# Performance work log

Hardware: AMD Instinct MI355X
Metric: run time of the kernel (lower is better)

Reference implementation:

```python
import jax, jax.numpy as jnp
import numpy as np

B, T, D, N = 16, 4096, 512, 3


def _window_sum(x, k):
    # x: [B, T, ...] -> sliding-window sum of size k, stride 1 -> [B, T-k+1, ...]
    c = jnp.cumsum(x, axis=1)
    c = jnp.concatenate([jnp.zeros_like(c[:, :1]), c], axis=1)
    return c[:, k:] - c[:, :-k]


def setup_inputs() -> dict:
    key = jax.random.key(0)
    ks = jax.random.split(key, 7)
    s_prev = jax.random.normal(ks[0], (B, D), jnp.float32)
    enc_hs = jax.random.normal(ks[1], (B, T, D), jnp.float32)
    # realistic padding mask: True = padded position
    lengths = jax.random.randint(ks[2], (B,), T // 2, T + 1)
    src_mask = jnp.arange(T)[None, :] >= lengths[:, None]
    scale = 1.0 / np.sqrt(D)
    Vw = jax.random.normal(ks[3], (N, D, D), jnp.float32) * scale
    Vb = jax.random.normal(ks[4], (N, D), jnp.float32) * 0.01
    Ww = jax.random.normal(ks[5], (N, D, D), jnp.float32) * scale
    Wb = jax.random.normal(ks[6], (N, D), jnp.float32) * 0.01
    return {"s_prev": s_prev, "enc_hs": enc_hs, "src_mask": src_mask,
            "Vw": Vw, "Vb": Vb, "Ww": Ww, "Wb": Wb}


def _level(s_prev, hs, mask, vw, vb, ww, wb):
    # hs: [B, L, D], mask: [B, L] (True = masked)
    # torch Linear: y = x @ W^T + b, weight is [out, in]
    v = jnp.einsum('bld,ed->ble', hs, vw) + vb            # V_i(hs)
    att = jnp.einsum('bd,bld->bl', s_prev, v)             # bmm(s_prev, V(hs)^T)
    att = jnp.where(mask, -jnp.inf, att)
    att = jax.nn.softmax(att, axis=-1)                    # [B, L]
    pooled = jnp.einsum('bl,bld->bd', att, hs)            # bmm(att, hs)
    ctx = pooled @ ww.T + wb                              # W_i(.)
    return ctx, att


def reference(s_prev, enc_hs, src_mask, Vw, Vb, Ww, Wb):
    ctx, att = _level(s_prev, enc_hs, src_mask, Vw[0], Vb[0], Ww[0], Wb[0])
    for i in range(1, N):
        k = i + 1
        hs_ngram = _window_sum(enc_hs, k) / k                      # AvgPool1d(k,1)
        n_mask = _window_sum(src_mask.astype(jnp.float32), k) > 0  # any masked in window
        c, _ = _level(s_prev, hs_ngram, n_mask, Vw[i], Vb[i], Ww[i], Wb[i])
        ctx = ctx + c
    return ctx, att
```

## Files before the change

### kernel.cpp

```cpp
#include <hip/hip_runtime.h>

#define BB 16
#define TT 4096
#define DD 512
#define CH 16
#define NY (TT/CH)
#define NEG (-1.0e30f)

#define OFF_Q     64
#define OFF_QP    (OFF_Q + 3*BB*DD)
#define OFF_P0    (OFF_QP + 4*3*BB*DD)
#define OFF_M     (OFF_P0 + BB*TT)
#define OFF_S     (OFF_M + 3*BB*NY)
#define OFF_SC    (OFF_S + 3*BB*NY)
#define OFF_MT    (OFF_SC + 3*BB*NY)
#define OFF_TOT   (OFF_MT + 64)
#define OFF_PART  (OFF_TOT + 64)
#define OFF_POOL  (OFF_PART + 3*NY*BB*DD)

__global__ void __launch_bounds__(1024) k_lengths(const unsigned char* mask, int* lengths) {
    __shared__ int sflag;
    const int tid = threadIdx.x;
    if (tid == 0) sflag = 0;
    __syncthreads();
    int f = 0;
    for (int idx = tid * 4 + 1; idx < BB * TT; idx += 1024 * 4)
        f |= (mask[idx] != 0);
    if (f) atomicOr(&sflag, 1);
    __syncthreads();
    const bool byte_layout = (sflag != 0);
    const int* m32 = (const int*)mask;
    const int b = tid >> 6;
    const int lane = tid & 63;
    int cnt = 0;
    if (byte_layout) {
        for (int t = lane; t < TT; t += 64) cnt += (mask[b * TT + t] != 0);
    } else {
        for (int t = lane; t < TT; t += 64) cnt += (m32[b * TT + t] != 0);
    }
    #pragma unroll
    for (int m = 32; m >= 1; m >>= 1) cnt += __shfl_xor(cnt, m, 64);
    if (lane == 0) lengths[b] = TT - cnt;
}

__global__ void __launch_bounds__(256) k_q(const float* __restrict__ s_prev,
                                           const float* __restrict__ Vw,
                                           float* __restrict__ qpart) {
    const int blk = blockIdx.x;
    const int ec = blk & 3;
    const int ib = blk >> 2;
    const int b = ib % BB;
    const int i = ib / BB;
    const int d0 = threadIdx.x;
    const float* sp = s_prev + b * DD + ec * 128;
    const float* W = Vw + (size_t)i * DD * DD + (size_t)(ec * 128) * DD;
    float a0 = 0.f, a1 = 0.f;
    for (int e = 0; e < 128; e++) {
        const float se = sp[e];
        a0 += se * W[e * DD + d0];
        a1 += se * W[e * DD + d0 + 256];
    }
    qpart[(size_t)blk * DD + d0] = a0;
    qpart[(size_t)blk * DD + d0 + 256] = a1;
}

__global__ void __launch_bounds__(256) k_q_reduce(const float* __restrict__ qpart,
                                                  float* __restrict__ q) {
    const int idx = blockIdx.x * 256 + threadIdx.x;
    const int ib = idx / DD;
    const int d = idx % DD;
    float s = 0.f;
    #pragma unroll
    for (int ec = 0; ec < 4; ec++) s += qpart[(size_t)(ib * 4 + ec) * DD + d];
    q[idx] = s;
}

__global__ void __launch_bounds__(256) k_fused(const float* __restrict__ enc,
                                               const float* __restrict__ q,
                                               const int* __restrict__ lengths,
                                               float* __restrict__ p0,
                                               float* __restrict__ mbuf,
                                               float* __restrict__ sbuf,
                                               float* __restrict__ part) {
    __shared__ float sp[CH + 2][3];
    __shared__ float svs[3][CH];
    __shared__ float su[3][CH];
    __shared__ float sm[3];
    const int b = blockIdx.x;
    const int y = blockIdx.y;
    const int t0 = y * CH;
    const int len = lengths[b];
    const int tid = threadIdx.x;
    if (t0 >= len) {
        if (tid < 3) {
            mbuf[(size_t)(tid * BB + b) * NY + y] = NEG;
            sbuf[(size_t)(tid * BB + b) * NY + y] = 0.f;
        }
        return;
    }
    const int wv = tid >> 6, lane = tid & 63;

    const float4* q40 = (const float4*)(q + (size_t)(0 * BB + b) * DD);
    const float4* q41 = (const float4*)(q + (size_t)(1 * BB + b) * DD);
    const float4* q42 = (const float4*)(q + (size_t)(2 * BB + b) * DD);
    const float4 qa0 = q40[lane], qb0 = q40[64 + lane];
    const float4 qa1 = q41[lane], qb1 = q41[64 + lane];
    const float4 qa2 = q42[lane], qb2 = q42[64 + lane];
    #pragma unroll
    for (int rr = 0; rr < 5; rr++) {
        if (rr == 4 && wv >= 2) break;
        const int r = (rr < 4) ? (wv + rr * 4) : (CH + wv);
        const int t = t0 + r;
        float d0 = 0.f, d1 = 0.f, d2 = 0.f;
        if (t < len) {
            const float4* e4 = (const float4*)(enc + ((size_t)b * TT + t) * DD);
            const float4 x0 = e4[lane], x1 = e4[64 + lane];
            d0 = x0.x*qa0.x + x0.y*qa0.y + x0.z*qa0.z + x0.w*qa0.w
               + x1.x*qb0.x + x1.y*qb0.y + x1.z*qb0.z + x1.w*qb0.w;
            d1 = x0.x*qa1.x + x0.y*qa1.y + x0.z*qa1.z + x0.w*qa1.w
               + x1.x*qb1.x + x1.y*qb1.y + x1.z*qb1.z + x1.w*qb1.w;
            d2 = x0.x*qa2.x + x0.y*qa2.y + x0.z*qa2.z + x0.w*qa2.w
               + x1.x*qb2.x + x1.y*qb2.y + x1.z*qb2.z + x1.w*qb2.w;
            #pragma unroll
            for (int m = 32; m >= 1; m >>= 1) {
                d0 += __shfl_xor(d0, m, 64);
                d1 += __shfl_xor(d1, m, 64);
                d2 += __shfl_xor(d2, m, 64);
            }
        }
        if (lane == 0) {
            sp[r][0] = d0; sp[r][1] = d1; sp[r][2] = d2;
            if (rr < 4 && t < len) p0[(size_t)b * TT + t] = d0;
        }
    }
    __syncthreads();

    if (tid < 48) {
        const int i = tid / CH, r = tid % CH;
        const int l = t0 + r;
        const bool valid = l < (len - i);
        float s = sp[r][i];
        if (i > 0) s += sp[r + 1][i];
        if (i > 1) s += sp[r + 2][i];
        svs[i][r] = valid ? s * (1.0f / (float)(i + 1)) : NEG;
    }
    __syncthreads();
    if (tid < 3) {
        float m = NEG;
        #pragma unroll
        for (int r = 0; r < CH; r++) m = fmaxf(m, svs[tid][r]);
        sm[tid] = m;
    }
    __syncthreads();
    if (tid < 48) {
        const int i = tid / CH, r = tid % CH;
        const bool valid = (t0 + r) < (len - i);
        su[i][r] = valid ? __expf(svs[i][r] - sm[i]) : 0.f;
    }
    __syncthreads();
    if (tid < 3) {
        float s = 0.f;
        #pragma unroll
        for (int r = 0; r < CH; r++) s += su[tid][r];
        mbuf[(size_t)(tid * BB + b) * NY + y] = sm[tid];
        sbuf[(size_t)(tid * BB + b) * NY + y] = s;
    }
    __syncthreads();

    const int d = tid * 2;
    const float* col = enc + (size_t)b * TT * DD + d;
    float2 va, vb2, vc;
    {
        const int t = t0;
        va  = (t     < TT) ? *(const float2*)(col + (size_t)t * DD)       : make_float2(0.f, 0.f);
        vb2 = (t + 1 < TT) ? *(const float2*)(col + (size_t)(t + 1) * DD) : make_float2(0.f, 0.f);
    }
    float2 a0 = {0, 0}, a1 = {0, 0}, a2 = {0, 0};
    #pragma unroll
    for (int r = 0; r < CH; r++) {
        const int t = t0 + r;
        vc = (t + 2 < TT) ? *(const float2*)(col + (size_t)(t + 2) * DD) : make_float2(0.f, 0.f);
        const float u0 = su[0][r], u1 = su[1][r], u2 = su[2][r];
        const float w1x = va.x + vb2.x, w1y = va.y + vb2.y;
        const float w2x = w1x + vc.x,   w2y = w1y + vc.y;
        a0.x += u0 * va.x;  a0.y += u0 * va.y;
        a1.x += u1 * w1x;   a1.y += u1 * w1y;
        a2.x += u2 * w2x;   a2.y += u2 * w2y;
        va = vb2; vb2 = vc;
    }
    a1.x *= 0.5f; a1.y *= 0.5f;
    a2.x *= (1.0f / 3.0f); a2.y *= (1.0f / 3.0f);
    float* pt = part + (size_t)y * BB * DD + (size_t)b * DD + d;
    *(float2*)(pt)                        = a0;
    *(float2*)(pt + (size_t)NY * BB * DD)     = a1;
    *(float2*)(pt + (size_t)2 * NY * BB * DD) = a2;
}

__global__ void __launch_bounds__(256) k_combine(const float* __restrict__ mbuf,
                                                 const float* __restrict__ sbuf,
                                                 float* __restrict__ scale,
                                                 float* __restrict__ mtot,
                                                 float* __restrict__ tot) {
    const int g = blockIdx.x * 4 + (threadIdx.x >> 6);
    const int lane = threadIdx.x & 63;
    const float* mv = mbuf + (size_t)g * NY;
    const float* sv = sbuf + (size_t)g * NY;
    float ml[4], sl[4];
    float m = NEG;
    #pragma unroll
    for (int j = 0; j < 4; j++) {
        ml[j] = mv[lane * 4 + j];
        sl[j] = sv[lane * 4 + j];
        m = fmaxf(m, ml[j]);
    }
    #pragma unroll
    for (int s = 32; s >= 1; s >>= 1) m = fmaxf(m, __shfl_xor(m, s, 64));
    float t = 0.f;
    #pragma unroll
    for (int j = 0; j < 4; j++) t += sl[j] * __expf(ml[j] - m);
    #pragma unroll
    for (int s = 32; s >= 1; s >>= 1) t += __shfl_xor(t, s, 64);
    const float inv = 1.0f / t;
    #pragma unroll
    for (int j = 0; j < 4; j++)
        scale[(size_t)g * NY + lane * 4 + j] = __expf(ml[j] - m) * inv;
    if (lane == 0) { mtot[g] = m; tot[g] = t; }
}

__global__ void __launch_bounds__(256) k_reduce(const float* __restrict__ part,
                                                const float* __restrict__ scale,
                                                float* __restrict__ pooled) {
    const int idx = blockIdx.x * 256 + threadIdx.x;
    const int ib = idx / DD;
    const int d = idx % DD;
    const int i = ib / BB, b = ib % BB;
    const float* sc = scale + (size_t)ib * NY;
    const float* base = part + (size_t)i * NY * BB * DD + (size_t)b * DD + d;
    float s = 0.f;
    #pragma unroll 8
    for (int y = 0; y < NY; y++) s += base[(size_t)y * BB * DD] * sc[y];
    pooled[idx] = s;
}

__global__ void __launch_bounds__(256) k_att(const float* __restrict__ p0,
                                             const int* __restrict__ lengths,
                                             const float* __restrict__ mtot,
                                             const float* __restrict__ tot,
                                             float* __restrict__ att) {
    const int idx = blockIdx.x * 256 + threadIdx.x;
    const int b = idx >> 12;
    const int t = idx & (TT - 1);
    const float m = mtot[b];
    const float inv = 1.0f / tot[b];
    att[idx] = (t < lengths[b]) ? __expf(p0[idx] - m) * inv : 0.f;
}

__global__ void __launch_bounds__(256) k_ctx(const float* __restrict__ pooled,
                                             const float* __restrict__ Ww,
                                             const float* __restrict__ Wb,
                                             float* __restrict__ ctx) {
    const int wid = blockIdx.x * 4 + (threadIdx.x >> 6);
    const int lane = threadIdx.x & 63;
    const int b = wid >> 9;
    const int e = wid & 511;
    float acc = 0.f;
    #pragma unroll
    for (int i = 0; i < 3; i++) {
        const float4* pr = (const float4*)(pooled + (size_t)(i * BB + b) * DD);
        const float4* wr = (const float4*)(Ww + ((size_t)i * DD + e) * DD);
        const float4 p0 = pr[lane], p1 = pr[64 + lane];
        const float4 w0 = wr[lane], w1 = wr[64 + lane];
        acc += p0.x * w0.x + p0.y * w0.y + p0.z * w0.z + p0.w * w0.w
             + p1.x * w1.x + p1.y * w1.y + p1.z * w1.z + p1.w * w1.w;
    }
    #pragma unroll
    for (int m = 32; m >= 1; m >>= 1) acc += __shfl_xor(acc, m, 64);
    if (lane == 0)
        ctx[(size_t)b * DD + e] = acc + Wb[e] + Wb[DD + e] + Wb[2 * DD + e];
}

extern "C" void kernel_launch(void* const* d_in, const int* in_sizes, int n_in,
                              void* d_out, int out_size, void* d_ws, size_t ws_size,
                              hipStream_t stream) {
    const float* s_prev = (const float*)d_in[0];
    const float* enc    = (const float*)d_in[1];
    const void*  mask   = d_in[2];
    const float* Vw     = (const float*)d_in[3];
    const float* Ww     = (const float*)d_in[5];
    const float* Wb     = (const float*)d_in[6];

    float* out = (float*)d_out;
    float* ctx = out;
    float* att = out + BB * DD;

    float* W       = (float*)d_ws;
    int*   lengths = (int*)d_ws;
    float* q       = W + OFF_Q;
    float* qpart   = W + OFF_QP;
    float* p0      = W + OFF_P0;
    float* mbuf    = W + OFF_M;
    float* sbuf    = W + OFF_S;
    float* scale   = W + OFF_SC;
    float* mtot    = W + OFF_MT;
    float* tot     = W + OFF_TOT;
    float* part    = W + OFF_PART;
    float* pooled  = W + OFF_POOL;

    k_lengths<<<1, 1024, 0, stream>>>((const unsigned char*)mask, lengths);
    k_q<<<192, 256, 0, stream>>>(s_prev, Vw, qpart);
    k_q_reduce<<<3 * BB * DD / 256, 256, 0, stream>>>(qpart, q);
    k_fused<<<dim3(BB, NY), 256, 0, stream>>>(enc, q, lengths, p0, mbuf, sbuf, part);
    k_combine<<<12, 256, 0, stream>>>(mbuf, sbuf, scale, mtot, tot);
    k_reduce<<<3 * BB * DD / 256, 256, 0, stream>>>(part, scale, pooled);
    k_att<<<BB * TT / 256, 256, 0, stream>>>(p0, lengths, mtot, tot, att);
    k_ctx<<<BB * DD / 4, 256, 0, stream>>>(pooled, Ww, Wb, ctx);
}
```

Before: 266.6 us.

## Enlarge chunk size, fuse softmax combine into reduce, merge small kernels

New measurement: 255.9 us. 4.0% less time.

```diff
diff --git a/kernel.cpp b/kernel.cpp
--- a/kernel.cpp
+++ b/kernel.cpp
@@ -3,89 +3,86 @@
 #define BB 16
 #define TT 4096
 #define DD 512
-#define CH 16
+#define CH 64
 #define NY (TT/CH)
 #define NEG (-1.0e30f)
 
 #define OFF_Q     64
-#define OFF_QP    (OFF_Q + 3*BB*DD)
-#define OFF_P0    (OFF_QP + 4*3*BB*DD)
+#define OFF_P0    (OFF_Q + 3*BB*DD)
 #define OFF_M     (OFF_P0 + BB*TT)
 #define OFF_S     (OFF_M + 3*BB*NY)
-#define OFF_SC    (OFF_S + 3*BB*NY)
-#define OFF_MT    (OFF_SC + 3*BB*NY)
+#define OFF_MT    (OFF_S + 3*BB*NY)
 #define OFF_TOT   (OFF_MT + 64)
 #define OFF_PART  (OFF_TOT + 64)
 #define OFF_POOL  (OFF_PART + 3*NY*BB*DD)
 
-__global__ void __launch_bounds__(1024) k_lengths(const unsigned char* mask, int* lengths) {
+__global__ void __launch_bounds__(256) k_lengths(const unsigned char* __restrict__ mask,
+                                                 int* __restrict__ lengths) {
     __shared__ int sflag;
+    __shared__ int wsum[4];
     const int tid = threadIdx.x;
+    const int b = blockIdx.x;
     if (tid == 0) sflag = 0;
     __syncthreads();
+    const uint4* m4 = (const uint4*)mask;
     int f = 0;
-    for (int idx = tid * 4 + 1; idx < BB * TT; idx += 1024 * 4)
-        f |= (mask[idx] != 0);
+    #pragma unroll 4
+    for (int idx = tid; idx < BB * TT / 16; idx += 256) {
+        const uint4 w = m4[idx];
+        f |= (((w.x | w.y | w.z | w.w) & 0xFFFFFF00u) != 0u);
+    }
     if (f) atomicOr(&sflag, 1);
     __syncthreads();
     const bool byte_layout = (sflag != 0);
     const int* m32 = (const int*)mask;
-    const int b = tid >> 6;
-    const int lane = tid & 63;
     int cnt = 0;
     if (byte_layout) {
-        for (int t = lane; t < TT; t += 64) cnt += (mask[b * TT + t] != 0);
+        for (int t = tid; t < TT; t += 256) cnt += (mask[b * TT + t] != 0);
     } else {
-        for (int t = lane; t < TT; t += 64) cnt += (m32[b * TT + t] != 0);
+        for (int t = tid; t < TT; t += 256) cnt += (m32[b * TT + t] != 0);
     }
     #pragma unroll
     for (int m = 32; m >= 1; m >>= 1) cnt += __shfl_xor(cnt, m, 64);
-    if (lane == 0) lengths[b] = TT - cnt;
-}
-
-__global__ void __launch_bounds__(256) k_q(const float* __restrict__ s_prev,
-                                           const float* __restrict__ Vw,
-                                           float* __restrict__ qpart) {
-    const int blk = blockIdx.x;
-    const int ec = blk & 3;
-    const int ib = blk >> 2;
+    if ((tid & 63) == 0) wsum[tid >> 6] = cnt;
+    __syncthreads();
+    if (tid == 0) lengths[b] = TT - (wsum[0] + wsum[1] + wsum[2] + wsum[3]);
+}
+
+__global__ void __launch_bounds__(1024) k_q(const float* __restrict__ s_prev,
+                                            const float* __restrict__ Vw,
+                                            float* __restrict__ q) {
+    __shared__ float red[4][DD];
+    const int ib = blockIdx.x;
     const int b = ib % BB;
     const int i = ib / BB;
-    const int d0 = threadIdx.x;
+    const int ec = threadIdx.x >> 8;
+    const int d0 = threadIdx.x & 255;
     const float* sp = s_prev + b * DD + ec * 128;
     const float* W = Vw + (size_t)i * DD * DD + (size_t)(ec * 128) * DD;
     float a0 = 0.f, a1 = 0.f;
+    #pragma unroll 4
     for (int e = 0; e < 128; e++) {
         const float se = sp[e];
         a0 += se * W[e * DD + d0];
         a1 += se * W[e * DD + d0 + 256];
     }
-    qpart[(size_t)blk * DD + d0] = a0;
-    qpart[(size_t)blk * DD + d0 + 256] = a1;
-}
-
-__global__ void __launch_bounds__(256) k_q_reduce(const float* __restrict__ qpart,
-                                                  float* __restrict__ q) {
-    const int idx = blockIdx.x * 256 + threadIdx.x;
-    const int ib = idx / DD;
-    const int d = idx % DD;
-    float s = 0.f;
-    #pragma unroll
-    for (int ec = 0; ec < 4; ec++) s += qpart[(size_t)(ib * 4 + ec) * DD + d];
-    q[idx] = s;
-}
-
-__global__ void __launch_bounds__(256) k_fused(const float* __restrict__ enc,
-                                               const float* __restrict__ q,
-                                               const int* __restrict__ lengths,
-                                               float* __restrict__ p0,
-                                               float* __restrict__ mbuf,
-                                               float* __restrict__ sbuf,
-                                               float* __restrict__ part) {
+    red[ec][d0] = a0;
+    red[ec][d0 + 256] = a1;
+    __syncthreads();
+    if (threadIdx.x < DD)
+        q[(size_t)ib * DD + threadIdx.x] = red[0][threadIdx.x] + red[1][threadIdx.x]
+                                         + red[2][threadIdx.x] + red[3][threadIdx.x];
+}
+
+__global__ void __launch_bounds__(512, 4) k_fused(const float* __restrict__ enc,
+                                                  const float* __restrict__ q,
+                                                  const int* __restrict__ lengths,
+                                                  float* __restrict__ p0,
+                                                  float* __restrict__ mbuf,
+                                                  float* __restrict__ sbuf,
+                                                  float* __restrict__ part) {
     __shared__ float sp[CH + 2][3];
-    __shared__ float svs[3][CH];
     __shared__ float su[3][CH];
-    __shared__ float sm[3];
     const int b = blockIdx.x;
     const int y = blockIdx.y;
     const int t0 = y * CH;
@@ -106,10 +103,8 @@
     const float4 qa0 = q40[lane], qb0 = q40[64 + lane];
     const float4 qa1 = q41[lane], qb1 = q41[64 + lane];
     const float4 qa2 = q42[lane], qb2 = q42[64 + lane];
-    #pragma unroll
-    for (int rr = 0; rr < 5; rr++) {
-        if (rr == 4 && wv >= 2) break;
-        const int r = (rr < 4) ? (wv + rr * 4) : (CH + wv);
+
+    auto row_task = [&](const int r, const bool wp0) {
         const int t = t0 + r;
         float d0 = 0.f, d1 = 0.f, d2 = 0.f;
         if (t < len) {
@@ -130,153 +125,128 @@
         }
         if (lane == 0) {
             sp[r][0] = d0; sp[r][1] = d1; sp[r][2] = d2;
-            if (rr < 4 && t < len) p0[(size_t)b * TT + t] = d0;
-        }
-    }
-    __syncthreads();
-
-    if (tid < 48) {
-        const int i = tid / CH, r = tid % CH;
+            if (wp0 && t < len) p0[(size_t)b * TT + t] = d0;
+        }
+    };
+    #pragma unroll 2
+    for (int rr = 0; rr < 8; rr++) row_task(wv + rr * 8, true);
+    if (wv < 2) row_task(CH + wv, false);
+    __syncthreads();
+
+    if (tid < 192) {
+        const int i = wv;
+        const int r = lane;
         const int l = t0 + r;
         const bool valid = l < (len - i);
         float s = sp[r][i];
         if (i > 0) s += sp[r + 1][i];
         if (i > 1) s += sp[r + 2][i];
-        svs[i][r] = valid ? s * (1.0f / (float)(i + 1)) : NEG;
-    }
-    __syncthreads();
-    if (tid < 3) {
-        float m = NEG;
-        #pragma unroll
-        for (int r = 0; r < CH; r++) m = fmaxf(m, svs[tid][r]);
-        sm[tid] = m;
-    }
-    __syncthreads();
-    if (tid < 48) {
-        const int i = tid / CH, r = tid % CH;
-        const bool valid = (t0 + r) < (len - i);
-        su[i][r] = valid ? __expf(svs[i][r] - sm[i]) : 0.f;
-    }
-    __syncthreads();
-    if (tid < 3) {
-        float s = 0.f;
-        #pragma unroll
-        for (int r = 0; r < CH; r++) s += su[tid][r];
-        mbuf[(size_t)(tid * BB + b) * NY + y] = sm[tid];
-        sbuf[(size_t)(tid * BB + b) * NY + y] = s;
-    }
-    __syncthreads();
-
-    const int d = tid * 2;
-    const float* col = enc + (size_t)b * TT * DD + d;
-    float2 va, vb2, vc;
-    {
-        const int t = t0;
-        va  = (t     < TT) ? *(const float2*)(col + (size_t)t * DD)       : make_float2(0.f, 0.f);
-        vb2 = (t + 1 < TT) ? *(const float2*)(col + (size_t)(t + 1) * DD) : make_float2(0.f, 0.f);
-    }
-    float2 a0 = {0, 0}, a1 = {0, 0}, a2 = {0, 0};
-    #pragma unroll
-    for (int r = 0; r < CH; r++) {
-        const int t = t0 + r;
-        vc = (t + 2 < TT) ? *(const float2*)(col + (size_t)(t + 2) * DD) : make_float2(0.f, 0.f);
-        const float u0 = su[0][r], u1 = su[1][r], u2 = su[2][r];
-        const float w1x = va.x + vb2.x, w1y = va.y + vb2.y;
-        const float w2x = w1x + vc.x,   w2y = w1y + vc.y;
-        a0.x += u0 * va.x;  a0.y += u0 * va.y;
-        a1.x += u1 * w1x;   a1.y += u1 * w1y;
-        a2.x += u2 * w2x;   a2.y += u2 * w2y;
+        const float kin = (i == 0) ? 1.0f : ((i == 1) ? 0.5f : (1.0f / 3.0f));
+        const float v = valid ? s * kin : NEG;
+        float m = v;
+        #pragma unroll
+        for (int mm = 32; mm >= 1; mm >>= 1) m = fmaxf(m, __shfl_xor(m, mm, 64));
+        const float u = valid ? __expf(v - m) : 0.f;
+        su[i][r] = u;
+        float ts = u;
+        #pragma unroll
+        for (int mm = 32; mm >= 1; mm >>= 1) ts += __shfl_xor(ts, mm, 64);
+        if (r == 0) {
+            mbuf[(size_t)(i * BB + b) * NY + y] = m;
+            sbuf[(size_t)(i * BB + b) * NY + y] = ts;
+        }
+    }
+    __syncthreads();
+
+    const float* col = enc + (size_t)b * TT * DD + tid;
+    float va = col[(size_t)t0 * DD];
+    float vb2 = (t0 + 1 < TT) ? col[(size_t)(t0 + 1) * DD] : 0.f;
+    float a0 = 0.f, a1 = 0.f, a2 = 0.f;
+    #pragma unroll 16
+    for (int rr = 0; rr < CH; rr++) {
+        const int t = t0 + rr;
+        const float vc = (t + 2 < TT) ? col[(size_t)(t + 2) * DD] : 0.f;
+        const float u0 = su[0][rr], u1 = su[1][rr], u2 = su[2][rr];
+        const float w1 = va + vb2;
+        const float w2 = w1 + vc;
+        a0 += u0 * va;
+        a1 += u1 * w1;
+        a2 += u2 * w2;
         va = vb2; vb2 = vc;
     }
-    a1.x *= 0.5f; a1.y *= 0.5f;
-    a2.x *= (1.0f / 3.0f); a2.y *= (1.0f / 3.0f);
-    float* pt = part + (size_t)y * BB * DD + (size_t)b * DD + d;
-    *(float2*)(pt)                        = a0;
-    *(float2*)(pt + (size_t)NY * BB * DD)     = a1;
-    *(float2*)(pt + (size_t)2 * NY * BB * DD) = a2;
-}
-
-__global__ void __launch_bounds__(256) k_combine(const float* __restrict__ mbuf,
-                                                 const float* __restrict__ sbuf,
-                                                 float* __restrict__ scale,
-                                                 float* __restrict__ mtot,
-                                                 float* __restrict__ tot) {
-    const int g = blockIdx.x * 4 + (threadIdx.x >> 6);
-    const int lane = threadIdx.x & 63;
-    const float* mv = mbuf + (size_t)g * NY;
-    const float* sv = sbuf + (size_t)g * NY;
-    float ml[4], sl[4];
-    float m = NEG;
-    #pragma unroll
-    for (int j = 0; j < 4; j++) {
-        ml[j] = mv[lane * 4 + j];
-        sl[j] = sv[lane * 4 + j];
-        m = fmaxf(m, ml[j]);
-    }
-    #pragma unroll
-    for (int s = 32; s >= 1; s >>= 1) m = fmaxf(m, __shfl_xor(m, s, 64));
-    float t = 0.f;
-    #pragma unroll
-    for (int j = 0; j < 4; j++) t += sl[j] * __expf(ml[j] - m);
-    #pragma unroll
-    for (int s = 32; s >= 1; s >>= 1) t += __shfl_xor(t, s, 64);
-    const float inv = 1.0f / t;
-    #pragma unroll
-    for (int j = 0; j < 4; j++)
-        scale[(size_t)g * NY + lane * 4 + j] = __expf(ml[j] - m) * inv;
-    if (lane == 0) { mtot[g] = m; tot[g] = t; }
+    a1 *= 0.5f; a2 *= (1.0f / 3.0f);
+    float* pt = part + (size_t)y * BB * DD + (size_t)b * DD + tid;
+    pt[0] = a0;
+    pt[(size_t)NY * BB * DD] = a1;
+    pt[(size_t)2 * NY * BB * DD] = a2;
 }
 
 __global__ void __launch_bounds__(256) k_reduce(const float* __restrict__ part,
-                                                const float* __restrict__ scale,
-                                                float* __restrict__ pooled) {
-    const int idx = blockIdx.x * 256 + threadIdx.x;
-    const int ib = idx / DD;
-    const int d = idx % DD;
+                                                const float* __restrict__ mbuf,
+                                                const float* __restrict__ sbuf,
+                                                float* __restrict__ pooled,
+                                                float* __restrict__ mtot,
+                                                float* __restrict__ tot) {
+    __shared__ float ssc[NY];
+    const int blk = blockIdx.x;
+    const int ib = blk >> 1;
+    const int d = ((blk & 1) << 8) + threadIdx.x;
     const int i = ib / BB, b = ib % BB;
-    const float* sc = scale + (size_t)ib * NY;
+    if (threadIdx.x < 64) {
+        const int lane = threadIdx.x;
+        const float ml = mbuf[(size_t)ib * NY + lane];
+        const float sl = sbuf[(size_t)ib * NY + lane];
+        float m = ml;
+        #pragma unroll
+        for (int s = 32; s >= 1; s >>= 1) m = fmaxf(m, __shfl_xor(m, s, 64));
+        float t = sl * __expf(ml - m);
+        #pragma unroll
+        for (int s = 32; s >= 1; s >>= 1) t += __shfl_xor(t, s, 64);
+        ssc[lane] = __expf(ml - m) / t;
+        if (lane == 0 && (blk & 1) == 0) { mtot[ib] = m; tot[ib] = t; }
+    }
+    __syncthreads();
     const float* base = part + (size_t)i * NY * BB * DD + (size_t)b * DD + d;
     float s = 0.f;
     #pragma unroll 8
-    for (int y = 0; y < NY; y++) s += base[(size_t)y * BB * DD] * sc[y];
-    pooled[idx] = s;
-}
-
-__global__ void __launch_bounds__(256) k_att(const float* __restrict__ p0,
+    for (int yy = 0; yy < NY; yy++) s += base[(size_t)yy * BB * DD] * ssc[yy];
+    pooled[(size_t)ib * DD + d] = s;
+}
+
+__global__ void __launch_bounds__(256) k_out(const float* __restrict__ pooled,
+                                             const float* __restrict__ Ww,
+                                             const float* __restrict__ Wb,
+                                             const float* __restrict__ p0,
                                              const int* __restrict__ lengths,
                                              const float* __restrict__ mtot,
                                              const float* __restrict__ tot,
+                                             float* __restrict__ ctx,
                                              float* __restrict__ att) {
-    const int idx = blockIdx.x * 256 + threadIdx.x;
-    const int b = idx >> 12;
-    const int t = idx & (TT - 1);
-    const float m = mtot[b];
-    const float inv = 1.0f / tot[b];
-    att[idx] = (t < lengths[b]) ? __expf(p0[idx] - m) * inv : 0.f;
-}
-
-__global__ void __launch_bounds__(256) k_ctx(const float* __restrict__ pooled,
-                                             const float* __restrict__ Ww,
-                                             const float* __restrict__ Wb,
-                                             float* __restrict__ ctx) {
-    const int wid = blockIdx.x * 4 + (threadIdx.x >> 6);
-    const int lane = threadIdx.x & 63;
-    const int b = wid >> 9;
-    const int e = wid & 511;
-    float acc = 0.f;
-    #pragma unroll
-    for (int i = 0; i < 3; i++) {
-        const float4* pr = (const float4*)(pooled + (size_t)(i * BB + b) * DD);
-        const float4* wr = (const float4*)(Ww + ((size_t)i * DD + e) * DD);
-        const float4 p0 = pr[lane], p1 = pr[64 + lane];
-        const float4 w0 = wr[lane], w1 = wr[64 + lane];
-        acc += p0.x * w0.x + p0.y * w0.y + p0.z * w0.z + p0.w * w0.w
-             + p1.x * w1.x + p1.y * w1.y + p1.z * w1.z + p1.w * w1.w;
-    }
-    #pragma unroll
-    for (int m = 32; m >= 1; m >>= 1) acc += __shfl_xor(acc, m, 64);
-    if (lane == 0)
-        ctx[(size_t)b * DD + e] = acc + Wb[e] + Wb[DD + e] + Wb[2 * DD + e];
+    if (blockIdx.x < BB * DD / 4) {
+        const int wid = blockIdx.x * 4 + (threadIdx.x >> 6);
+        const int lane = threadIdx.x & 63;
+        const int b = wid >> 9;
+        const int e = wid & 511;
+        float acc = 0.f;
+        #pragma unroll
+        for (int i = 0; i < 3; i++) {
+            const float4* pr = (const float4*)(pooled + (size_t)(i * BB + b) * DD);
+            const float4* wr = (const float4*)(Ww + ((size_t)i * DD + e) * DD);
+            const float4 pA = pr[lane], pB = pr[64 + lane];
+            const float4 wA = wr[lane], wB = wr[64 + lane];
+            acc += pA.x * wA.x + pA.y * wA.y + pA.z * wA.z + pA.w * wA.w
+                 + pB.x * wB.x + pB.y * wB.y + pB.z * wB.z + pB.w * wB.w;
+        }
+        #pragma unroll
+        for (int m = 32; m >= 1; m >>= 1) acc += __shfl_xor(acc, m, 64);
+        if (lane == 0)
+            ctx[(size_t)b * DD + e] = acc + Wb[e] + Wb[DD + e] + Wb[2 * DD + e];
+    } else {
+        const int idx = (blockIdx.x - BB * DD / 4) * 256 + threadIdx.x;
+        const int b = idx >> 12;
+        const int t = idx & (TT - 1);
+        att[idx] = (t < lengths[b]) ? __expf(p0[idx] - mtot[b]) * (1.0f / tot[b]) : 0.f;
+    }
 }
 
 extern "C" void kernel_launch(void* const* d_in, const int* in_sizes, int n_in,
@@ -296,22 +266,18 @@
     float* W       = (float*)d_ws;
     int*   lengths = (int*)d_ws;
     float* q       = W + OFF_Q;
-    float* qpart   = W + OFF_QP;
     float* p0      = W + OFF_P0;
     float* mbuf    = W + OFF_M;
     float* sbuf    = W + OFF_S;
-    float* scale   = W + OFF_SC;
     float* mtot    = W + OFF_MT;
     float* tot     = W + OFF_TOT;
     float* part    = W + OFF_PART;
     float* pooled  = W + OFF_POOL;
 
-    k_lengths<<<1, 1024, 0, stream>>>((const unsigned char*)mask, lengths);
-    k_q<<<192, 256, 0, stream>>>(s_prev, Vw, qpart);
-    k_q_reduce<<<3 * BB * DD / 256, 256, 0, stream>>>(qpart, q);
-    k_fused<<<dim3(BB, NY), 256, 0, stream>>>(enc, q, lengths, p0, mbuf, sbuf, part);
-    k_combine<<<12, 256, 0, stream>>>(mbuf, sbuf, scale, mtot, tot);
-    k_reduce<<<3 * BB * DD / 256, 256, 0, stream>>>(part, scale, pooled);
-    k_att<<<BB * TT / 256, 256, 0, stream>>>(p0, lengths, mtot, tot, att);
-    k_ctx<<<BB * DD / 4, 256, 0, stream>>>(pooled, Ww, Wb, ctx);
-}
+    k_lengths<<<BB, 256, 0, stream>>>((const unsigned char*)mask, lengths);
+    k_q<<<48, 1024, 0, stream>>>(s_prev, Vw, q);
+    k_fused<<<dim3(BB, NY), 512, 0, stream>>>(enc, q, lengths, p0, mbuf, sbuf, part);
+    k_reduce<<<96, 256, 0, stream>>>(part, mbuf, sbuf, pooled, mtot, tot);
+    k_out<<<BB * DD / 4 + BB * TT / 256, 256, 0, stream>>>(pooled, Ww, Wb, p0, lengths,
+                                                           mtot, tot, ctx, att);
+}
```
